# Performance work log

Hardware: AMD Instinct MI355X
Metric: run time of the kernel (lower is better)

Reference implementation:

```python
import jax, jax.numpy as jnp
import numpy as np
import math

B, S, E = 4, 2048, 1024

def setup_inputs() -> dict:
    key = jax.random.key(0)
    ks = jax.random.split(key, 12)
    scale = 1.0 / math.sqrt(E)
    inp = {
        "query": jax.random.normal(ks[0], (B, S, E), jnp.float32),
        "key_": jax.random.normal(ks[1], (B, S, E), jnp.float32),
        "value": jax.random.normal(ks[2], (B, S, E), jnp.float32),
        # causal mask, broadcast over batch: 1 = keep, 0 = mask
        "mask": jnp.broadcast_to(jnp.tril(jnp.ones((S, S), jnp.int32)), (B, S, S)),
        "Wq": jax.random.uniform(ks[3], (E, E), jnp.float32, -scale, scale),
        "bq": jax.random.uniform(ks[4], (E,), jnp.float32, -scale, scale),
        "Wk": jax.random.uniform(ks[5], (E, E), jnp.float32, -scale, scale),
        "bk": jax.random.uniform(ks[6], (E,), jnp.float32, -scale, scale),
        "Wv": jax.random.uniform(ks[7], (E, E), jnp.float32, -scale, scale),
        "bv": jax.random.uniform(ks[8], (E,), jnp.float32, -scale, scale),
        "Wo": jax.random.uniform(ks[9], (E, E), jnp.float32, -scale, scale),
        "bo": jax.random.uniform(ks[10], (E,), jnp.float32, -scale, scale),
    }
    return inp

def reference(query, key_, value, mask, Wq, bq, Wk, bk, Wv, bv, Wo, bo):
    # Linear projections (torch Linear: x @ W.T + b)
    Q = jnp.einsum('bse,fe->bsf', query, Wq) + bq
    K = jnp.einsum('bse,fe->bsf', key_, Wk) + bk
    V = jnp.einsum('bse,fe->bsf', value, Wv) + bv
    # NOTE: module never splits heads; scores over full embed_dim, scaled by sqrt(embed_dim)
    scores = jnp.einsum('bqe,bke->bqk', Q, K) / jnp.sqrt(jnp.asarray(E, Q.dtype))
    scores = jnp.where(mask == 0, -jnp.inf, scores)
    attn = jax.nn.softmax(scores, axis=-1)
    attn_out = jnp.einsum('bqk,bke->bqe', attn, V)
    return jnp.einsum('bse,fe->bsf', attn_out, Wo) + bo
```

## Files before the change

### kernel.cpp

```cpp
#include <hip/hip_runtime.h>

typedef __bf16 bf16;
typedef __attribute__((ext_vector_type(8))) __bf16 bf16x8;
typedef __attribute__((ext_vector_type(4))) __bf16 bf16x4;
typedef __attribute__((ext_vector_type(2))) __bf16 bf16x2;
typedef __attribute__((ext_vector_type(4))) float f32x4;

#define DEVINL __device__ __forceinline__

DEVINL void gload_lds16(const bf16* g, bf16* l) {
    __builtin_amdgcn_global_load_lds(
        (__attribute__((address_space(1))) unsigned int*)(unsigned long long)g,
        (__attribute__((address_space(3))) unsigned int*)l,
        16, 0, 0);
}

DEVINL void xcd_swizzle(int& bx, int& by) {
    const int gx = gridDim.x, gy = gridDim.y;
    const int l = blockIdx.y * gx + blockIdx.x;
    const int xcd = l & 7;
    const int li = l >> 3;
    by = xcd * (gy >> 3) + li / gx;
    bx = li - (li / gx) * gx;
}

DEVINL void xcd_swizzle_bal(int& bx, int& by) {
    const int gx = gridDim.x, gy = gridDim.y;
    const int l = blockIdx.y * gx + blockIdx.x;
    const int xcd = l & 7;
    const int li = l >> 3;
    const int j = li / gx;
    bx = li - j * gx;
    by = j ? (gy - 1 - xcd) : xcd;
}

__global__ __launch_bounds__(256) void cvt3_f32_to_bf16(
    const float* __restrict__ a, const float* __restrict__ b,
    const float* __restrict__ c, bf16* __restrict__ out, int n4) {
    int i = blockIdx.x * blockDim.x + threadIdx.x;
    if (i >= n4) return;
    const float* src = (blockIdx.z == 0) ? a : (blockIdx.z == 1) ? b : c;
    bf16* dst = out + (size_t)blockIdx.z * (size_t)n4 * 4;
    float4 f = ((const float4*)src)[i];
    bf16x4 o;
    o.x = (bf16)f.x; o.y = (bf16)f.y; o.z = (bf16)f.z; o.w = (bf16)f.w;
    ((bf16x4*)dst)[i] = o;
}

__global__ __launch_bounds__(256) void cvt4_f32_to_bf16(
    const float* __restrict__ a, const float* __restrict__ b,
    const float* __restrict__ c, const float* __restrict__ d,
    bf16* __restrict__ out, int n4) {
    int i = blockIdx.x * blockDim.x + threadIdx.x;
    if (i >= n4) return;
    const float* src = (blockIdx.z == 0) ? a : (blockIdx.z == 1) ? b
                     : (blockIdx.z == 2) ? c : d;
    bf16* dst = out + (size_t)blockIdx.z * (size_t)n4 * 4;
    float4 f = ((const float4*)src)[i];
    bf16x4 o;
    o.x = (bf16)f.x; o.y = (bf16)f.y; o.z = (bf16)f.z; o.w = (bf16)f.w;
    ((bf16x4*)dst)[i] = o;
}

__global__ __launch_bounds__(256) void transpose_bf16(
    const unsigned short* __restrict__ in, unsigned short* __restrict__ out,
    int R, int C) {
    __shared__ unsigned short t[64][65];
    const size_t bo = (size_t)blockIdx.z * R * C;
    const int r0 = blockIdx.y * 64, c0 = blockIdx.x * 64;
#pragma unroll
    for (int i = 0; i < 16; i++) {
        int lin = threadIdx.x + i * 256;
        int r = lin >> 6, c = lin & 63;
        t[r][c] = in[bo + (size_t)(r0 + r) * C + (c0 + c)];
    }
    __syncthreads();
#pragma unroll
    for (int i = 0; i < 16; i++) {
        int lin = threadIdx.x + i * 256;
        int r = lin >> 6, c = lin & 63;
        out[bo + (size_t)(c0 + r) * R + (r0 + c)] = t[c][r];
    }
}

__global__ __launch_bounds__(256) void bias_fold(
    const float* __restrict__ Wo, const float* __restrict__ bv,
    const float* __restrict__ bo, float* __restrict__ bout) {
    const int e = blockIdx.x * 4 + (threadIdx.x >> 6);
    const int lane = threadIdx.x & 63;
    float s = 0.f;
    for (int k = lane; k < 1024; k += 64) s += Wo[e * 1024 + k] * bv[k];
#pragma unroll
    for (int off = 32; off > 0; off >>= 1) s += __shfl_xor(s, off, 64);
    if (lane == 0) bout[e] = s + bo[e];
}

template <int EPI>
__global__ __launch_bounds__(256) void gemm_bt128(
    const bf16* __restrict__ A, const bf16* __restrict__ B,
    const float* __restrict__ bias0, const float* __restrict__ bias1,
    const float* __restrict__ bias2, void* __restrict__ Cv,
    int M, int N, int K,
    long long sA, long long sB, long long sC,
    float scale) {
    int bx, by;
    xcd_swizzle(bx, by);
    const int bz = blockIdx.z;
    const int m0 = by * 128, n0 = bx * 128;

    A += (size_t)bz * sA;
    B += (size_t)bz * sB;
    const float* bias = (bz == 0) ? bias0 : (bz == 1) ? bias1 : bias2;

    __shared__ __align__(16) bf16 As[2][128 * 32];
    __shared__ __align__(16) bf16 Bs[2][128 * 32];

    const int tid = threadIdx.x;
    const int wave = tid >> 6;
    const int lane = tid & 63;
    const int lr = lane & 15;
    const int lq = lane >> 4;
    const int wm = (wave >> 1) * 64;
    const int wn = (wave & 1) * 64;
    const int srow = lane >> 2;
    const int scol = ((lane & 3) ^ ((lane >> 3) & 3)) * 8;

    const bf16* gA = A + (size_t)(m0 + wave * 16 + srow) * K + scol;
    const bf16* gB = B + (size_t)(n0 + wave * 16 + srow) * K + scol;
    const size_t rowskip = (size_t)64 * K;
    const int rsw = (lq ^ ((lr >> 1) & 3)) * 8;

    f32x4 acc[4][4];
    const f32x4 fzero = {0.f, 0.f, 0.f, 0.f};
#pragma unroll
    for (int i = 0; i < 4; i++)
#pragma unroll
        for (int j = 0; j < 4; j++) acc[i][j] = fzero;

#define STAGE128(bufi)                                          \
    do {                                                        \
        gload_lds16(gA,           As[bufi] + wave * 512);       \
        gload_lds16(gA + rowskip, As[bufi] + (wave + 4) * 512); \
        gload_lds16(gB,           Bs[bufi] + wave * 512);       \
        gload_lds16(gB + rowskip, Bs[bufi] + (wave + 4) * 512); \
        gA += 32; gB += 32;                                     \
    } while (0)

    STAGE128(0);
    int cur = 0;
    for (int k0 = 0; k0 < K; k0 += 32) {
        __syncthreads();
        if (k0 + 32 < K) STAGE128(cur ^ 1);

        bf16x8 af[4], bfr[4];
#pragma unroll
        for (int i = 0; i < 4; i++)
            af[i] = *(const bf16x8*)(As[cur] + (wm + i * 16 + lr) * 32 + rsw);
#pragma unroll
        for (int j = 0; j < 4; j++)
            bfr[j] = *(const bf16x8*)(Bs[cur] + (wn + j * 16 + lr) * 32 + rsw);
#pragma unroll
        for (int i = 0; i < 4; i++)
#pragma unroll
            for (int j = 0; j < 4; j++)
                acc[i][j] = __builtin_amdgcn_mfma_f32_16x16x32_bf16(
                    af[i], bfr[j], acc[i][j], 0, 0, 0);
        cur ^= 1;
    }
#undef STAGE128

#pragma unroll
    for (int j = 0; j < 4; j++) {
        const int col = n0 + wn + j * 16 + lr;
        const float bb = bias ? bias[col] : 0.0f;
#pragma unroll
        for (int i = 0; i < 4; i++) {
            const int rowb = m0 + wm + i * 16 + lq * 4;
#pragma unroll
            for (int r = 0; r < 4; r++) {
                if (EPI == 0)
                    ((bf16*)Cv)[(size_t)bz * sC + (size_t)(rowb + r) * N + col] =
                        (bf16)(acc[i][j][r] * scale + bb);
                else
                    ((float*)Cv)[(size_t)bz * sC + (size_t)(rowb + r) * N + col] =
                        acc[i][j][r] * scale + bb;
            }
        }
    }
}

template <int EPI>
__global__ __launch_bounds__(256) void gemm_bt64(
    const bf16* __restrict__ A, const bf16* __restrict__ B,
    const float* __restrict__ bias, void* __restrict__ Cv,
    int M, int N, int K,
    long long sA, long long sB, long long sC,
    float scale, int causal) {
    int bx, by;
    if (causal) xcd_swizzle_bal(bx, by);
    else        xcd_swizzle(bx, by);
    const int bz = blockIdx.z;
    const int m0 = by * 128, n0 = bx * 64;
    if (causal == 1 && n0 > m0 + 127) return;
    int Keff = K;
    if (causal == 2) { Keff = m0 + 128; if (Keff > K) Keff = K; }

    A += (size_t)bz * sA;
    B += (size_t)bz * sB;

    __shared__ __align__(16) bf16 As[2][128 * 32];
    __shared__ __align__(16) bf16 Bs[2][64 * 32];

    const int tid = threadIdx.x;
    const int wave = tid >> 6;
    const int lane = tid & 63;
    const int lr = lane & 15;
    const int lq = lane >> 4;
    const int wm = wave * 32;
    const int srow = lane >> 2;
    const int scol = ((lane & 3) ^ ((lane >> 3) & 3)) * 8;

    const bf16* gA = A + (size_t)(m0 + wave * 16 + srow) * K + scol;
    const bf16* gB = B + (size_t)(n0 + wave * 16 + srow) * K + scol;
    const size_t rowskip = (size_t)64 * K;
    const int rsw = (lq ^ ((lr >> 1) & 3)) * 8;

    f32x4 acc[2][4];
    const f32x4 fzero = {0.f, 0.f, 0.f, 0.f};
#pragma unroll
    for (int i = 0; i < 2; i++)
#pragma unroll
        for (int j = 0; j < 4; j++) acc[i][j] = fzero;

#define STAGE64(bufi)                                           \
    do {                                                        \
        gload_lds16(gA,           As[bufi] + wave * 512);       \
        gload_lds16(gA + rowskip, As[bufi] + (wave + 4) * 512); \
        gload_lds16(gB,           Bs[bufi] + wave * 512);       \
        gA += 32; gB += 32;                                     \
    } while (0)

    STAGE64(0);
    int cur = 0;
    for (int k0 = 0; k0 < Keff; k0 += 32) {
        __syncthreads();
        if (k0 + 32 < Keff) STAGE64(cur ^ 1);

        bf16x8 af[2], bfr[4];
#pragma unroll
        for (int i = 0; i < 2; i++)
            af[i] = *(const bf16x8*)(As[cur] + (wm + i * 16 + lr) * 32 + rsw);
#pragma unroll
        for (int j = 0; j < 4; j++)
            bfr[j] = *(const bf16x8*)(Bs[cur] + (j * 16 + lr) * 32 + rsw);
#pragma unroll
        for (int i = 0; i < 2; i++)
#pragma unroll
            for (int j = 0; j < 4; j++)
                acc[i][j] = __builtin_amdgcn_mfma_f32_16x16x32_bf16(
                    af[i], bfr[j], acc[i][j], 0, 0, 0);
        cur ^= 1;
    }
#undef STAGE64

#pragma unroll
    for (int j = 0; j < 4; j++) {
        const int col = n0 + j * 16 + lr;
        const float bb = bias ? bias[col] : 0.0f;
#pragma unroll
        for (int i = 0; i < 2; i++) {
            const int rowb = m0 + wm + i * 16 + lq * 4;
#pragma unroll
            for (int r = 0; r < 4; r++) {
                if (EPI == 0)
                    ((bf16*)Cv)[(size_t)bz * sC + (size_t)(rowb + r) * N + col] =
                        (bf16)(acc[i][j][r] * scale + bb);
                else
                    ((float*)Cv)[(size_t)bz * sC + (size_t)(rowb + r) * N + col] =
                        acc[i][j][r] * scale + bb;
            }
        }
    }
}

__global__ __launch_bounds__(256) void softmax_causal(
    const bf16* __restrict__ Sc, bf16* __restrict__ P, int S) {
    const int row = blockIdx.x;
    const int q = row & (S - 1);
    const bf16* src = Sc + (size_t)row * S;
    bf16* dst = P + (size_t)row * S;
    const int L = q + 1;
    const int tid = threadIdx.x;

    float v[8];
    float mx = -3.0e38f;
#pragma unroll
    for (int i = 0; i < 4; i++) {
        int k = (i * 256 + tid) * 2;
        bf16x2 u = ((const bf16x2*)src)[i * 256 + tid];
        v[2 * i]     = (k < L)     ? (float)u.x : -3.0e38f;
        v[2 * i + 1] = (k + 1 < L) ? (float)u.y : -3.0e38f;
        mx = fmaxf(mx, fmaxf(v[2 * i], v[2 * i + 1]));
    }
#pragma unroll
    for (int off = 32; off > 0; off >>= 1) mx = fmaxf(mx, __shfl_xor(mx, off, 64));
    __shared__ float redm[4], reds[4];
    if ((tid & 63) == 0) redm[tid >> 6] = mx;
    __syncthreads();
    mx = fmaxf(fmaxf(redm[0], redm[1]), fmaxf(redm[2], redm[3]));

    float sum = 0.f;
#pragma unroll
    for (int i = 0; i < 8; i++) {
        float e = (v[i] > -1.0e38f) ? __expf(v[i] - mx) : 0.f;
        v[i] = e;
        sum += e;
    }
#pragma unroll
    for (int off = 32; off > 0; off >>= 1) sum += __shfl_xor(sum, off, 64);
    if ((tid & 63) == 0) reds[tid >> 6] = sum;
    __syncthreads();
    sum = reds[0] + reds[1] + reds[2] + reds[3];
    const float inv = 1.0f / sum;
#pragma unroll
    for (int i = 0; i < 4; i++) {
        bf16x2 o;
        o.x = (bf16)(v[2 * i] * inv);
        o.y = (bf16)(v[2 * i + 1] * inv);
        ((bf16x2*)dst)[i * 256 + tid] = o;
    }
}

extern "C" void kernel_launch(void* const* d_in, const int* in_sizes, int n_in,
                              void* d_out, int out_size, void* d_ws, size_t ws_size,
                              hipStream_t stream) {
    const int B = 4, S = 2048, E = 1024;
    const size_t SBE = (size_t)B * S * E;
    const size_t EE = (size_t)E * E;

    const float* q_in = (const float*)d_in[0];
    const float* k_in = (const float*)d_in[1];
    const float* v_in = (const float*)d_in[2];
    const float* Wq = (const float*)d_in[4];
    const float* bq = (const float*)d_in[5];
    const float* Wk = (const float*)d_in[6];
    const float* bk = (const float*)d_in[7];
    const float* Wv = (const float*)d_in[8];
    const float* bv = (const float*)d_in[9];
    const float* Wo = (const float*)d_in[10];
    const float* bo = (const float*)d_in[11];

    char* ws = (char*)d_ws;
    bf16* qkvb = (bf16*)ws;
    bf16* Sc = (bf16*)ws;
    bf16* WvT = (bf16*)(ws + 3 * SBE * 2);
    float* bout = (float*)(ws + 3 * SBE * 2 + EE * 2);
    char* p = ws + (size_t)B * S * S * 4;
    bf16* QKVb = (bf16*)p; p += 3 * SBE * 2;
    bf16* VWt = (bf16*)p; p += SBE * 2;
    bf16* Pb = (bf16*)p; p += (size_t)B * S * S * 2;
    bf16* Wb = (bf16*)p; p += 4 * EE * 2;

    bf16* Qb = QKVb;
    bf16* Kb = QKVb + SBE;
    bf16* VW = QKVb + 2 * SBE;
    bf16* Wob = Wb + 3 * EE;
    bf16* Wvo = Wb + 2 * EE;

    dim3 blk(256);

    dim3 gcvt3((int)(SBE / 4 / 256), 1, 3);
    cvt3_f32_to_bf16<<<gcvt3, blk, 0, stream>>>(q_in, k_in, v_in, qkvb, (int)(SBE / 4));
    dim3 gcvt4((int)(EE / 4 / 256), 1, 4);
    cvt4_f32_to_bf16<<<gcvt4, blk, 0, stream>>>(Wq, Wk, Wv, Wo, Wb, (int)(EE / 4));

    dim3 gtw(16, 16, 1);
    transpose_bf16<<<gtw, blk, 0, stream>>>((const unsigned short*)(Wb + 2 * EE),
                                            (unsigned short*)WvT, E, E);
    dim3 gwvo(E / 128, E / 128, 1);
    gemm_bt128<0><<<gwvo, blk, 0, stream>>>(Wob, WvT, nullptr, nullptr, nullptr,
                                            Wvo, E, E, E, 0, 0, 0, 1.f);
    bias_fold<<<256, blk, 0, stream>>>(Wo, bv, bo, bout);

    dim3 gproj(E / 128, (B * S) / 128, 3);
    gemm_bt128<0><<<gproj, blk, 0, stream>>>(qkvb, Wb, bq, bk, nullptr, QKVb,
                                             B * S, E, E,
                                             (long long)SBE, (long long)EE,
                                             (long long)SBE, 1.f);

    dim3 gt(E / 64, S / 64, B);
    transpose_bf16<<<gt, blk, 0, stream>>>((const unsigned short*)VW,
                                           (unsigned short*)VWt, S, E);

    dim3 gsc(S / 64, S / 128, B);
    gemm_bt64<0><<<gsc, blk, 0, stream>>>(Qb, Kb, nullptr, Sc, S, S, E,
                                          (long long)S * E, (long long)S * E,
                                          (long long)S * S, 0.03125f, 1);

    softmax_causal<<<B * S, blk, 0, stream>>>(Sc, Pb, S);

    dim3 gpv(E / 64, S / 128, B);
    gemm_bt64<1><<<gpv, blk, 0, stream>>>(Pb, VWt, bout, (float*)d_out, S, E, S,
                                          (long long)S * S, (long long)E * S,
                                          (long long)S * E, 1.f, 2);
}
```

Measured before the change: 403.5 us.

## Replace 128x64 GEMMs with 512-thread 128x256 four-stage pipelined GEMM

Adds a new GEMM kernel with 8 waves and a 128x256 output tile per block. It keeps four LDS stages of A and B filled through global_load_lds, uses explicit vmcnt waits and raw barriers, and raises wave priority around the MFMA block. The aim is to hide global-load latency and get more operand reuse per LDS read. The kernel replaces the QKV projection, the score GEMM and the PV GEMM. The PV GEMM no longer uses the causal K truncation, so it now runs the full K range over zero probabilities, which adds work.

```diff
diff --git a/kernel.cpp b/kernel.cpp
--- a/kernel.cpp
+++ b/kernel.cpp
@@ -190,9 +190,10 @@
 }
 
 template <int EPI>
-__global__ __launch_bounds__(256) void gemm_bt64(
+__global__ __launch_bounds__(512) void gemm_pipe(
     const bf16* __restrict__ A, const bf16* __restrict__ B,
-    const float* __restrict__ bias, void* __restrict__ Cv,
+    const float* __restrict__ bias0, const float* __restrict__ bias1,
+    const float* __restrict__ bias2, void* __restrict__ Cv,
     int M, int N, int K,
     long long sA, long long sB, long long sC,
     float scale, int causal) {
@@ -200,75 +201,93 @@
     if (causal) xcd_swizzle_bal(bx, by);
     else        xcd_swizzle(bx, by);
     const int bz = blockIdx.z;
-    const int m0 = by * 128, n0 = bx * 64;
+    const int m0 = by * 128, n0 = bx * 256;
     if (causal == 1 && n0 > m0 + 127) return;
     int Keff = K;
     if (causal == 2) { Keff = m0 + 128; if (Keff > K) Keff = K; }
+    const int NT = Keff >> 5;
 
     A += (size_t)bz * sA;
     B += (size_t)bz * sB;
-
-    __shared__ __align__(16) bf16 As[2][128 * 32];
-    __shared__ __align__(16) bf16 Bs[2][64 * 32];
+    const float* bias = (bz == 0) ? bias0 : (bz == 1) ? bias1 : bias2;
+
+    __shared__ __align__(16) bf16 As[4][128 * 32];
+    __shared__ __align__(16) bf16 Bs[4][256 * 32];
 
     const int tid = threadIdx.x;
     const int wave = tid >> 6;
     const int lane = tid & 63;
     const int lr = lane & 15;
     const int lq = lane >> 4;
-    const int wm = wave * 32;
+    const int wm = (wave >> 2) * 64;
+    const int wn = (wave & 3) * 64;
+
     const int srow = lane >> 2;
     const int scol = ((lane & 3) ^ ((lane >> 3) & 3)) * 8;
-
-    const bf16* gA = A + (size_t)(m0 + wave * 16 + srow) * K + scol;
-    const bf16* gB = B + (size_t)(n0 + wave * 16 + srow) * K + scol;
-    const size_t rowskip = (size_t)64 * K;
+    const bf16* gA  = A + (size_t)(m0 + wave * 16 + srow) * K + scol;
+    const bf16* gB0 = B + (size_t)(n0 + wave * 32 + srow) * K + scol;
+    const size_t rowskip = (size_t)16 * K;
+
     const int rsw = (lq ^ ((lr >> 1) & 3)) * 8;
 
-    f32x4 acc[2][4];
+    f32x4 acc[4][4];
     const f32x4 fzero = {0.f, 0.f, 0.f, 0.f};
 #pragma unroll
-    for (int i = 0; i < 2; i++)
+    for (int i = 0; i < 4; i++)
 #pragma unroll
         for (int j = 0; j < 4; j++) acc[i][j] = fzero;
 
-#define STAGE64(bufi)                                           \
-    do {                                                        \
-        gload_lds16(gA,           As[bufi] + wave * 512);       \
-        gload_lds16(gA + rowskip, As[bufi] + (wave + 4) * 512); \
-        gload_lds16(gB,           Bs[bufi] + wave * 512);       \
-        gA += 32; gB += 32;                                     \
+#define STAGEP(bufi, koff)                                               \
+    do {                                                                 \
+        gload_lds16(gA + (koff),            As[bufi] + wave * 512);      \
+        gload_lds16(gB0 + (koff),           Bs[bufi] + wave * 1024);     \
+        gload_lds16(gB0 + rowskip + (koff), Bs[bufi] + wave * 1024 + 512); \
     } while (0)
 
-    STAGE64(0);
-    int cur = 0;
-    for (int k0 = 0; k0 < Keff; k0 += 32) {
-        __syncthreads();
-        if (k0 + 32 < Keff) STAGE64(cur ^ 1);
-
-        bf16x8 af[2], bfr[4];
-#pragma unroll
-        for (int i = 0; i < 2; i++)
-            af[i] = *(const bf16x8*)(As[cur] + (wm + i * 16 + lr) * 32 + rsw);
+    if (NT > 0) STAGEP(0, 0);
+    if (NT > 1) STAGEP(1, 32);
+    if (NT > 2) STAGEP(2, 64);
+    if (NT > 2)      asm volatile("s_waitcnt vmcnt(6)" ::: "memory");
+    else if (NT > 1) asm volatile("s_waitcnt vmcnt(3)" ::: "memory");
+    else             asm volatile("s_waitcnt vmcnt(0)" ::: "memory");
+    __builtin_amdgcn_s_barrier();
+
+    for (int t = 0; t < NT; ++t) {
+        const int bfi = t & 3;
+
+        bf16x8 af[4], bfr[4];
+#pragma unroll
+        for (int i = 0; i < 4; i++)
+            af[i] = *(const bf16x8*)(As[bfi] + (wm + i * 16 + lr) * 32 + rsw);
 #pragma unroll
         for (int j = 0; j < 4; j++)
-            bfr[j] = *(const bf16x8*)(Bs[cur] + (j * 16 + lr) * 32 + rsw);
-#pragma unroll
-        for (int i = 0; i < 2; i++)
+            bfr[j] = *(const bf16x8*)(Bs[bfi] + (wn + j * 16 + lr) * 32 + rsw);
+
+        if (t + 3 < NT) STAGEP((t + 3) & 3, (t + 3) * 32);
+
+        if (t + 3 < NT)      asm volatile("s_waitcnt vmcnt(6)" ::: "memory");
+        else if (t + 2 < NT) asm volatile("s_waitcnt vmcnt(3)" ::: "memory");
+        else                 asm volatile("s_waitcnt vmcnt(0)" ::: "memory");
+        __builtin_amdgcn_s_barrier();
+
+        __builtin_amdgcn_s_setprio(1);
+#pragma unroll
+        for (int i = 0; i < 4; i++)
 #pragma unroll
             for (int j = 0; j < 4; j++)
                 acc[i][j] = __builtin_amdgcn_mfma_f32_16x16x32_bf16(
                     af[i], bfr[j], acc[i][j], 0, 0, 0);
-        cur ^= 1;
-    }
-#undef STAGE64
+        __builtin_amdgcn_s_setprio(0);
+        __builtin_amdgcn_s_barrier();
+    }
+#undef STAGEP
 
 #pragma unroll
     for (int j = 0; j < 4; j++) {
-        const int col = n0 + j * 16 + lr;
+        const int col = n0 + wn + j * 16 + lr;
         const float bb = bias ? bias[col] : 0.0f;
 #pragma unroll
-        for (int i = 0; i < 2; i++) {
+        for (int i = 0; i < 4; i++) {
             const int rowb = m0 + wm + i * 16 + lq * 4;
 #pragma unroll
             for (int r = 0; r < 4; r++) {
@@ -367,7 +386,7 @@
     bf16* Wob = Wb + 3 * EE;
     bf16* Wvo = Wb + 2 * EE;
 
-    dim3 blk(256);
+    dim3 blk(256), blk512(512);
 
     dim3 gcvt3((int)(SBE / 4 / 256), 1, 3);
     cvt3_f32_to_bf16<<<gcvt3, blk, 0, stream>>>(q_in, k_in, v_in, qkvb, (int)(SBE / 4));
@@ -382,25 +401,27 @@
                                             Wvo, E, E, E, 0, 0, 0, 1.f);
     bias_fold<<<256, blk, 0, stream>>>(Wo, bv, bo, bout);
 
-    dim3 gproj(E / 128, (B * S) / 128, 3);
-    gemm_bt128<0><<<gproj, blk, 0, stream>>>(qkvb, Wb, bq, bk, nullptr, QKVb,
-                                             B * S, E, E,
-                                             (long long)SBE, (long long)EE,
-                                             (long long)SBE, 1.f);
+    dim3 gproj(E / 256, (B * S) / 128, 3);
+    gemm_pipe<0><<<gproj, blk512, 0, stream>>>(qkvb, Wb, bq, bk, nullptr, QKVb,
+                                               B * S, E, E,
+                                               (long long)SBE, (long long)EE,
+                                               (long long)SBE, 1.f, 0);
 
     dim3 gt(E / 64, S / 64, B);
     transpose_bf16<<<gt, blk, 0, stream>>>((const unsigned short*)VW,
                                            (unsigned short*)VWt, S, E);
 
-    dim3 gsc(S / 64, S / 128, B);
-    gemm_bt64<0><<<gsc, blk, 0, stream>>>(Qb, Kb, nullptr, Sc, S, S, E,
-                                          (long long)S * E, (long long)S * E,
-                                          (long long)S * S, 0.03125f, 1);
+    dim3 gsc(S / 256, S / 128, B);
+    gemm_pipe<0><<<gsc, blk512, 0, stream>>>(Qb, Kb, nullptr, nullptr, nullptr, Sc,
+                                             S, S, E,
+                                             (long long)S * E, (long long)S * E,
+                                             (long long)S * S, 0.03125f, 1);
 
     softmax_causal<<<B * S, blk, 0, stream>>>(Sc, Pb, S);
 
-    dim3 gpv(E / 64, S / 128, B);
-    gemm_bt64<1><<<gpv, blk, 0, stream>>>(Pb, VWt, bout, (float*)d_out, S, E, S,
-                                          (long long)S * S, (long long)E * S,
-                                          (long long)S * E, 1.f, 2);
-}
+    dim3 gpv(E / 256, S / 128, B);
+    gemm_pipe<1><<<gpv, blk512, 0, stream>>>(Pb, VWt, bout, bout, bout,
+                                             (float*)d_out, S, E, S,
+                                             (long long)S * S, (long long)E * S,
+                                             (long long)S * E, 1.f, 0);
+}
```

New measurement: 398.7 us. About the same (-1.2%).
